# Kernel tuning notes

Hardware: AMD Instinct MI355X
Metric: run time of the kernel (lower is better)

## Reference

```python
import jax, jax.numpy as jnp
import numpy as np

SEQ, BATCH, IN_CH = 4096, 8, 256
HID = 256
LOOKBACK, LOOKAHEAD = 1, 0
K = LOOKBACK + 1 + LOOKAHEAD  # conv kernel size = 2


def setup_inputs() -> dict:
    key = jax.random.key(0)
    k1, k2, k3, k4, k5, k6 = jax.random.split(key, 6)
    X = jax.random.normal(k1, (SEQ, BATCH, IN_CH), dtype=jnp.float32)
    hidden = jax.random.normal(k2, (BATCH, HID), dtype=jnp.float32)
    scale = 1.0 / np.sqrt(IN_CH * K)
    Wz = jax.random.normal(k3, (HID, IN_CH, K), dtype=jnp.float32) * scale
    bz = jax.random.normal(k4, (HID,), dtype=jnp.float32) * scale
    Wf = jax.random.normal(k5, (HID, IN_CH, K), dtype=jnp.float32) * scale
    bf = jax.random.normal(k6, (HID,), dtype=jnp.float32) * scale
    return {"X": X, "hidden": hidden, "Wz": Wz, "bz": bz, "Wf": Wf, "bf": bf}


def _conv1d(Xp, W, b):
    # Xp: (B, C_in, S_pad); W: (C_out, C_in, K) -> (B, C_out, S)
    y = jax.lax.conv_general_dilated(
        Xp, W, window_strides=(1,), padding='VALID',
        dimension_numbers=('NCW', 'OIW', 'NCW'))
    return y + b[None, :, None]


def reference(X, hidden, Wz, bz, Wf, bf):
    # pad seq dim: lookback zeros in front, lookahead behind
    X_pad = jnp.pad(X, ((LOOKBACK, LOOKAHEAD), (0, 0), (0, 0)))
    Xp = jnp.transpose(X_pad, (1, 2, 0))  # (B, C_in, S_pad)

    Z = jnp.transpose(_conv1d(Xp, Wz, bz), (2, 0, 1))  # (S, B, H)
    F = jnp.transpose(_conv1d(Xp, Wf, bf), (2, 0, 1))  # (S, B, H)

    Z = Z * jax.nn.sigmoid(1.702 * Z)  # QuickGELU
    F = jax.nn.sigmoid(F)

    def step(h, fz):
        f, z = fz
        h = f * z + (1.0 - f) * h
        return h, h

    h_last, H = jax.lax.scan(step, hidden, (F, Z))
    return H, h_last[None]  # (S,B,H), (1,B,H)
```

## Files before the change

### kernel.cpp

```cpp
#include <hip/hip_runtime.h>


#define SEQn 4096
#define NCH 2048
#define CHUNK 32
#define NCHUNK 128

typedef __attribute__((ext_vector_type(8))) short bf16x8;
typedef __attribute__((ext_vector_type(4))) float floatx4;

__device__ __forceinline__ unsigned short f2bf(float x) {
  unsigned int u = __float_as_uint(x);
  u += 0x7fffu + ((u >> 16) & 1u);
  return (unsigned short)(u >> 16);
}
__device__ __forceinline__ float bf2f(ushort u) {
  return __uint_as_float((unsigned int)u << 16);
}
__device__ __forceinline__ float sigf(float x) {
  return __builtin_amdgcn_rcpf(1.0f + __expf(-x));
}

__global__ void pack_kernel(const float* __restrict__ X,
                            const float* __restrict__ Wz, const float* __restrict__ Wf,
                            ushort* __restrict__ Xbf, ushort* __restrict__ Bm) {
  if (blockIdx.x < 1024) {
    int idx = blockIdx.x * 256 + threadIdx.x;
    int n = idx >> 9, kin = idx & 511;
    const float* W = (n < 256) ? Wz : Wf;
    int h = n & 255, c = kin & 255, tap = kin >> 8;
    Bm[idx] = f2bf(W[h * 512 + c * 2 + tap]);
  } else {
    int idx = (blockIdx.x - 1024) * 256 + threadIdx.x;
    const int total4 = ((SEQn + 1) * NCH) / 4;
    if (idx >= total4) return;
    const int pad4 = NCH / 4;
    float4 v;
    if (idx < pad4) { v.x = 0.f; v.y = 0.f; v.z = 0.f; v.w = 0.f; }
    else v = ((const float4*)X)[idx - pad4];
    ushort4 o;
    o.x = f2bf(v.x); o.y = f2bf(v.y); o.z = f2bf(v.z); o.w = f2bf(v.w);
    ((ushort4*)Xbf)[idx] = o;
  }
}

__global__ __launch_bounds__(256) void gemm_kernel(
    const ushort* __restrict__ Xbf, const ushort* __restrict__ Bm,
    const float* __restrict__ bz, const float* __restrict__ bfb,
    ushort* __restrict__ zout, ushort* __restrict__ fout) {
  __shared__ __align__(16) char smem_raw[32768];
  ushort* sA = (ushort*)smem_raw;
  ushort* sB = (ushort*)(smem_raw + 16384);
  ushort* sT = (ushort*)smem_raw;

  const int tid  = threadIdx.x;
  const int wave = tid >> 6;
  const int lane = tid & 63;
  const int quad = lane >> 4;
  const int lrow = lane & 15;
  const int wm = wave >> 1;
  const int wn = wave & 1;
  const int bm = blockIdx.x;
  const int bn = blockIdx.y;

  floatx4 acc[4][4];
#pragma unroll
  for (int i = 0; i < 4; ++i)
#pragma unroll
    for (int j = 0; j < 4; ++j)
      acc[i][j] = (floatx4){0.f, 0.f, 0.f, 0.f};

  int rowS[4], gko[4];
#pragma unroll
  for (int it = 0; it < 4; ++it) {
    int g = wave * 256 + it * 64 + lane;
    int row = g >> 3, ks8 = g & 7;
    rowS[it] = row;
    gko[it] = (ks8 ^ (row & 7)) * 8;
  }
  char* ldsA = (char*)sA + wave * 4096 + (lane << 4);
  char* ldsB = (char*)sB + wave * 4096 + (lane << 4);

  for (int k0 = 0; k0 < 512; k0 += 64) {
    __syncthreads();
#pragma unroll
    for (int it = 0; it < 4; ++it) {
      const int kk = k0 + gko[it];
      const int cA = (kk < 256) ? kk : kk + 1792;
      __builtin_amdgcn_global_load_lds(
          (const __attribute__((address_space(1))) void*)(Xbf + (size_t)(bm * 128 + rowS[it]) * 256 + cA),
          (__attribute__((address_space(3))) void*)(ldsA + it * 1024), 16, 0, 0);
      __builtin_amdgcn_global_load_lds(
          (const __attribute__((address_space(1))) void*)(Bm + (size_t)(bn * 128 + rowS[it]) * 512 + kk),
          (__attribute__((address_space(3))) void*)(ldsB + it * 1024), 16, 0, 0);
    }
    __syncthreads();

    bf16x8 af[4][2], bfr[4][2];
#pragma unroll
    for (int fi = 0; fi < 4; ++fi) {
      const int r = wm * 64 + fi * 16 + lrow;
#pragma unroll
      for (int ks = 0; ks < 2; ++ks) {
        const int s = (ks * 4 + quad) ^ (r & 7);
        af[fi][ks] = *(const bf16x8*)&sA[r * 64 + s * 8];
      }
    }
#pragma unroll
    for (int fj = 0; fj < 4; ++fj) {
      const int r = wn * 64 + fj * 16 + lrow;
#pragma unroll
      for (int ks = 0; ks < 2; ++ks) {
        const int s = (ks * 4 + quad) ^ (r & 7);
        bfr[fj][ks] = *(const bf16x8*)&sB[r * 64 + s * 8];
      }
    }
#pragma unroll
    for (int ks = 0; ks < 2; ++ks)
#pragma unroll
      for (int fi = 0; fi < 4; ++fi)
#pragma unroll
        for (int fj = 0; fj < 4; ++fj)
          acc[fi][fj] = __builtin_amdgcn_mfma_f32_16x16x32_bf16(af[fi][ks], bfr[fj][ks], acc[fi][fj], 0, 0, 0);
  }

  const bool isZ = (bn < 2);
  ushort* gout = isZ ? zout : fout;
  const int ncol0 = (bn & 1) * 128;
  const float* bias = isZ ? bz : bfb;
  float bv[4];
#pragma unroll
  for (int fj = 0; fj < 4; ++fj)
    bv[fj] = bias[ncol0 + wn * 64 + fj * 16 + lrow];

  for (int round = 0; round < 2; ++round) {
    __syncthreads();
    if (wm == round) {
#pragma unroll
      for (int fi = 0; fi < 4; ++fi)
#pragma unroll
        for (int fj = 0; fj < 4; ++fj)
#pragma unroll
          for (int r = 0; r < 4; ++r) {
            float v = acc[fi][fj][r] + bv[fj];
            float o = isZ ? (v * sigf(1.702f * v)) : sigf(v);
            sT[(fi * 16 + quad * 4 + r) * 136 + wn * 64 + fj * 16 + lrow] = f2bf(o);
          }
    }
    __syncthreads();
#pragma unroll
    for (int it = 0; it < 4; ++it) {
      int e = tid + it * 256;
      int row = e >> 4, seg = e & 15;
      uint4 v = *(uint4*)&sT[row * 136 + seg * 8];
      *(uint4*)(gout + (size_t)(bm * 128 + round * 64 + row) * 256 + ncol0 + seg * 8) = v;
    }
  }
}

__global__ void scanA_kernel(const ushort* __restrict__ z, const ushort* __restrict__ f,
                             float* __restrict__ Ac, float* __restrict__ Cc) {
  int t = blockIdx.x * blockDim.x + threadIdx.x;
  int ch2 = t & 1023;
  int j = t >> 10;
  const size_t base = (size_t)j * CHUNK * NCH + 2 * ch2;
  const ushort* zp = z + base;
  const ushort* fp = f + base;
  float A0 = 1.0f, C0 = 0.0f, A1 = 1.0f, C1 = 0.0f;
#pragma unroll
  for (int i = 0; i < CHUNK; ++i) {
    ushort2 fv = *(const ushort2*)(fp + (size_t)i * NCH);
    ushort2 zv = *(const ushort2*)(zp + (size_t)i * NCH);
    float f0 = bf2f(fv.x), f1 = bf2f(fv.y);
    float a0 = 1.0f - f0, a1 = 1.0f - f1;
    C0 = fmaf(a0, C0, f0 * bf2f(zv.x)); A0 *= a0;
    C1 = fmaf(a1, C1, f1 * bf2f(zv.y)); A1 *= a1;
  }
  float2 Av = {A0, A1}, Cv = {C0, C1};
  *(float2*)(Ac + (size_t)j * NCH + 2 * ch2) = Av;
  *(float2*)(Cc + (size_t)j * NCH + 2 * ch2) = Cv;
}

__global__ void scanB_kernel(const float* __restrict__ hidden,
                             const float* __restrict__ Ac, const float* __restrict__ Cc,
                             float* __restrict__ Hs) {
  const int lane = threadIdx.x & 63;
  const int ch = blockIdx.x * 4 + (threadIdx.x >> 6);
  const int j0 = 2 * lane, j1 = 2 * lane + 1;
  float a0 = Ac[j0 * NCH + ch], c0 = Cc[j0 * NCH + ch];
  float a1 = Ac[j1 * NCH + ch], c1 = Cc[j1 * NCH + ch];
  float a = a0 * a1;
  float c = fmaf(a1, c0, c1);
#pragma unroll
  for (int d = 1; d < 64; d <<= 1) {
    float pa = __shfl_up(a, d, 64);
    float pc = __shfl_up(c, d, 64);
    if (lane >= d) { c = fmaf(a, pc, c); a *= pa; }
  }
  float xa = __shfl_up(a, 1, 64), xc = __shfl_up(c, 1, 64);
  if (lane == 0) { xa = 1.0f; xc = 0.0f; }
  float h0 = hidden[ch];
  float hs0 = fmaf(xa, h0, xc);
  Hs[j0 * NCH + ch] = hs0;
  Hs[j1 * NCH + ch] = fmaf(a0, hs0, c0);
}

__global__ void scanC_kernel(const ushort* __restrict__ z, const ushort* __restrict__ f,
                             const float* __restrict__ Hs, float* __restrict__ out) {
  int t = blockIdx.x * blockDim.x + threadIdx.x;
  int ch2 = t & 1023;
  int j = t >> 10;
  float2 hv = *(const float2*)(Hs + (size_t)j * NCH + 2 * ch2);
  float h0 = hv.x, h1 = hv.y;
  const size_t base = (size_t)j * CHUNK * NCH + 2 * ch2;
  const ushort* zp = z + base;
  const ushort* fp = f + base;
  float* op = out + base;
#pragma unroll
  for (int i = 0; i < CHUNK; ++i) {
    ushort2 fv = *(const ushort2*)(fp + (size_t)i * NCH);
    ushort2 zv = *(const ushort2*)(zp + (size_t)i * NCH);
    float f0 = bf2f(fv.x), f1 = bf2f(fv.y);
    h0 = fmaf(f0, bf2f(zv.x) - h0, h0);
    h1 = fmaf(f1, bf2f(zv.y) - h1, h1);
    float2 o = {h0, h1};
    *(float2*)(op + (size_t)i * NCH) = o;
  }
  if (j == NCHUNK - 1) {
    float2 o = {h0, h1};
    *(float2*)(out + (size_t)SEQn * NCH + 2 * ch2) = o;
  }
}

extern "C" void kernel_launch(void* const* d_in, const int* in_sizes, int n_in,
                              void* d_out, int out_size, void* d_ws, size_t ws_size,
                              hipStream_t stream) {
  const float* X      = (const float*)d_in[0];
  const float* hidden = (const float*)d_in[1];
  const float* Wz     = (const float*)d_in[2];
  const float* bz     = (const float*)d_in[3];
  const float* Wf     = (const float*)d_in[4];
  const float* bfb    = (const float*)d_in[5];
  float* out = (float*)d_out;

  char* ws = (char*)d_ws;
  ushort* zbf = (ushort*)ws;
  ushort* fbf = (ushort*)(ws + 16777216);
  ushort* Xbf = (ushort*)(ws + 33554432);
  ushort* Bm  = (ushort*)(ws + 50335744);
  float* Ac = (float*)(ws + 33554432);
  float* Cc = (float*)(ws + 34603008);
  float* Hs = (float*)(ws + 35651584);

  pack_kernel<<<9218, 256, 0, stream>>>(X, Wz, Wf, Xbf, Bm);
  dim3 ggrid(256, 4);
  gemm_kernel<<<ggrid, 256, 0, stream>>>(Xbf, Bm, bz, bfb, zbf, fbf);
  scanA_kernel<<<512, 256, 0, stream>>>(zbf, fbf, Ac, Cc);
  scanB_kernel<<<512, 256, 0, stream>>>(hidden, Ac, Cc, Hs);
  scanC_kernel<<<512, 256, 0, stream>>>(zbf, fbf, Hs, out);
}
```

Measured before the change: 144.4 us.

## Fuse three scan passes into one persistent kernel with grid barriers

Merges the chunk-reduce, cross-chunk prefix, and chunk-apply scan kernels into a single 512-block kernel separated by atomic grid-wide barriers. The z/f values for each chunk stay in registers between the first and third phases, so they are not re-read from global memory, and two kernel launches are removed. The risks are higher register pressure from the 64 cached words, barrier spin overhead, and a possible deadlock if all 512 blocks cannot be co-resident. The barrier counter is reset inside the pack kernel.

```diff
diff --git a/kernel.cpp b/kernel.cpp
--- a/kernel.cpp
+++ b/kernel.cpp
@@ -5,6 +5,7 @@
 #define NCH 2048
 #define CHUNK 32
 #define NCHUNK 128
+#define NBLK_SCAN 512
 
 typedef __attribute__((ext_vector_type(8))) short bf16x8;
 typedef __attribute__((ext_vector_type(4))) float floatx4;
@@ -17,13 +18,35 @@
 __device__ __forceinline__ float bf2f(ushort u) {
   return __uint_as_float((unsigned int)u << 16);
 }
+__device__ __forceinline__ float bf2f_lo(unsigned int v) {
+  return __uint_as_float(v << 16);
+}
+__device__ __forceinline__ float bf2f_hi(unsigned int v) {
+  return __uint_as_float(v & 0xffff0000u);
+}
 __device__ __forceinline__ float sigf(float x) {
   return __builtin_amdgcn_rcpf(1.0f + __expf(-x));
 }
 
+__device__ __forceinline__ void grid_bar(unsigned int* bar, unsigned int target) {
+  __syncthreads();
+  if (threadIdx.x == 0) {
+    __threadfence();
+    __hip_atomic_fetch_add(bar, 1u, __ATOMIC_RELEASE, __HIP_MEMORY_SCOPE_AGENT);
+    while (__hip_atomic_load(bar, __ATOMIC_ACQUIRE, __HIP_MEMORY_SCOPE_AGENT) < target) {
+      __builtin_amdgcn_s_sleep(2);
+    }
+    __threadfence();
+  }
+  __syncthreads();
+}
+
 __global__ void pack_kernel(const float* __restrict__ X,
                             const float* __restrict__ Wz, const float* __restrict__ Wf,
-                            ushort* __restrict__ Xbf, ushort* __restrict__ Bm) {
+                            ushort* __restrict__ Xbf, ushort* __restrict__ Bm,
+                            unsigned int* __restrict__ bar) {
+  if (blockIdx.x == 0 && threadIdx.x == 0)
+    __hip_atomic_store(bar, 0u, __ATOMIC_RELAXED, __HIP_MEMORY_SCOPE_AGENT);
   if (blockIdx.x < 1024) {
     int idx = blockIdx.x * 256 + threadIdx.x;
     int n = idx >> 9, kin = idx & 511;
@@ -158,77 +181,77 @@
   }
 }
 
-__global__ void scanA_kernel(const ushort* __restrict__ z, const ushort* __restrict__ f,
-                             float* __restrict__ Ac, float* __restrict__ Cc) {
-  int t = blockIdx.x * blockDim.x + threadIdx.x;
-  int ch2 = t & 1023;
-  int j = t >> 10;
+__global__ __launch_bounds__(256, 2) void scan_fused(
+    const float* __restrict__ hidden,
+    const ushort* __restrict__ z, const ushort* __restrict__ f,
+    float* __restrict__ Ac, float* __restrict__ Cc, float* __restrict__ Hs,
+    float* __restrict__ out, unsigned int* __restrict__ bar) {
+  const int t = blockIdx.x * 256 + threadIdx.x;
+  const int ch2 = t & 1023;
+  const int j = t >> 10;
   const size_t base = (size_t)j * CHUNK * NCH + 2 * ch2;
-  const ushort* zp = z + base;
-  const ushort* fp = f + base;
+
+  unsigned int zreg[CHUNK], freg[CHUNK];
   float A0 = 1.0f, C0 = 0.0f, A1 = 1.0f, C1 = 0.0f;
 #pragma unroll
   for (int i = 0; i < CHUNK; ++i) {
-    ushort2 fv = *(const ushort2*)(fp + (size_t)i * NCH);
-    ushort2 zv = *(const ushort2*)(zp + (size_t)i * NCH);
-    float f0 = bf2f(fv.x), f1 = bf2f(fv.y);
+    unsigned int fv = *(const unsigned int*)(f + base + (size_t)i * NCH);
+    unsigned int zv = *(const unsigned int*)(z + base + (size_t)i * NCH);
+    freg[i] = fv; zreg[i] = zv;
+    float f0 = bf2f_lo(fv), f1 = bf2f_hi(fv);
     float a0 = 1.0f - f0, a1 = 1.0f - f1;
-    C0 = fmaf(a0, C0, f0 * bf2f(zv.x)); A0 *= a0;
-    C1 = fmaf(a1, C1, f1 * bf2f(zv.y)); A1 *= a1;
-  }
-  float2 Av = {A0, A1}, Cv = {C0, C1};
-  *(float2*)(Ac + (size_t)j * NCH + 2 * ch2) = Av;
-  *(float2*)(Cc + (size_t)j * NCH + 2 * ch2) = Cv;
-}
-
-__global__ void scanB_kernel(const float* __restrict__ hidden,
-                             const float* __restrict__ Ac, const float* __restrict__ Cc,
-                             float* __restrict__ Hs) {
-  const int lane = threadIdx.x & 63;
-  const int ch = blockIdx.x * 4 + (threadIdx.x >> 6);
-  const int j0 = 2 * lane, j1 = 2 * lane + 1;
-  float a0 = Ac[j0 * NCH + ch], c0 = Cc[j0 * NCH + ch];
-  float a1 = Ac[j1 * NCH + ch], c1 = Cc[j1 * NCH + ch];
-  float a = a0 * a1;
-  float c = fmaf(a1, c0, c1);
-#pragma unroll
-  for (int d = 1; d < 64; d <<= 1) {
-    float pa = __shfl_up(a, d, 64);
-    float pc = __shfl_up(c, d, 64);
-    if (lane >= d) { c = fmaf(a, pc, c); a *= pa; }
-  }
-  float xa = __shfl_up(a, 1, 64), xc = __shfl_up(c, 1, 64);
-  if (lane == 0) { xa = 1.0f; xc = 0.0f; }
-  float h0 = hidden[ch];
-  float hs0 = fmaf(xa, h0, xc);
-  Hs[j0 * NCH + ch] = hs0;
-  Hs[j1 * NCH + ch] = fmaf(a0, hs0, c0);
-}
-
-__global__ void scanC_kernel(const ushort* __restrict__ z, const ushort* __restrict__ f,
-                             const float* __restrict__ Hs, float* __restrict__ out) {
-  int t = blockIdx.x * blockDim.x + threadIdx.x;
-  int ch2 = t & 1023;
-  int j = t >> 10;
-  float2 hv = *(const float2*)(Hs + (size_t)j * NCH + 2 * ch2);
-  float h0 = hv.x, h1 = hv.y;
-  const size_t base = (size_t)j * CHUNK * NCH + 2 * ch2;
-  const ushort* zp = z + base;
-  const ushort* fp = f + base;
-  float* op = out + base;
-#pragma unroll
-  for (int i = 0; i < CHUNK; ++i) {
-    ushort2 fv = *(const ushort2*)(fp + (size_t)i * NCH);
-    ushort2 zv = *(const ushort2*)(zp + (size_t)i * NCH);
-    float f0 = bf2f(fv.x), f1 = bf2f(fv.y);
-    h0 = fmaf(f0, bf2f(zv.x) - h0, h0);
-    h1 = fmaf(f1, bf2f(zv.y) - h1, h1);
-    float2 o = {h0, h1};
-    *(float2*)(op + (size_t)i * NCH) = o;
-  }
-  if (j == NCHUNK - 1) {
-    float2 o = {h0, h1};
-    *(float2*)(out + (size_t)SEQn * NCH + 2 * ch2) = o;
+    C0 = fmaf(a0, C0, f0 * bf2f_lo(zv)); A0 *= a0;
+    C1 = fmaf(a1, C1, f1 * bf2f_hi(zv)); A1 *= a1;
+  }
+  {
+    float2 Av = {A0, A1}, Cv = {C0, C1};
+    *(float2*)(Ac + (size_t)j * NCH + 2 * ch2) = Av;
+    *(float2*)(Cc + (size_t)j * NCH + 2 * ch2) = Cv;
+  }
+
+  grid_bar(bar, NBLK_SCAN);
+
+  {
+    const int lane = threadIdx.x & 63;
+    const int ch = blockIdx.x * 4 + (threadIdx.x >> 6);
+    const int j0 = 2 * lane, j1 = 2 * lane + 1;
+    float a0 = Ac[j0 * NCH + ch], c0 = Cc[j0 * NCH + ch];
+    float a1 = Ac[j1 * NCH + ch], c1 = Cc[j1 * NCH + ch];
+    float a = a0 * a1;
+    float c = fmaf(a1, c0, c1);
+#pragma unroll
+    for (int d = 1; d < 64; d <<= 1) {
+      float pa = __shfl_up(a, d, 64);
+      float pc = __shfl_up(c, d, 64);
+      if (lane >= d) { c = fmaf(a, pc, c); a *= pa; }
+    }
+    float xa = __shfl_up(a, 1, 64), xc = __shfl_up(c, 1, 64);
+    if (lane == 0) { xa = 1.0f; xc = 0.0f; }
+    float h0 = hidden[ch];
+    float hs0 = fmaf(xa, h0, xc);
+    Hs[j0 * NCH + ch] = hs0;
+    Hs[j1 * NCH + ch] = fmaf(a0, hs0, c0);
+  }
+
+  grid_bar(bar, 2 * NBLK_SCAN);
+
+  {
+    float2 hv = *(const float2*)(Hs + (size_t)j * NCH + 2 * ch2);
+    float h0 = hv.x, h1 = hv.y;
+    float* op = out + base;
+#pragma unroll
+    for (int i = 0; i < CHUNK; ++i) {
+      unsigned int fv = freg[i], zv = zreg[i];
+      float f0 = bf2f_lo(fv), f1 = bf2f_hi(fv);
+      h0 = fmaf(f0, bf2f_lo(zv) - h0, h0);
+      h1 = fmaf(f1, bf2f_hi(zv) - h1, h1);
+      float2 o = {h0, h1};
+      *(float2*)(op + (size_t)i * NCH) = o;
+    }
+    if (j == NCHUNK - 1) {
+      float2 o = {h0, h1};
+      *(float2*)(out + (size_t)SEQn * NCH + 2 * ch2) = o;
+    }
   }
 }
 
@@ -248,14 +271,13 @@
   ushort* fbf = (ushort*)(ws + 16777216);
   ushort* Xbf = (ushort*)(ws + 33554432);
   ushort* Bm  = (ushort*)(ws + 50335744);
+  unsigned int* bar = (unsigned int*)(ws + 50860032);
   float* Ac = (float*)(ws + 33554432);
   float* Cc = (float*)(ws + 34603008);
   float* Hs = (float*)(ws + 35651584);
 
-  pack_kernel<<<9218, 256, 0, stream>>>(X, Wz, Wf, Xbf, Bm);
+  pack_kernel<<<9218, 256, 0, stream>>>(X, Wz, Wf, Xbf, Bm, bar);
   dim3 ggrid(256, 4);
   gemm_kernel<<<ggrid, 256, 0, stream>>>(Xbf, Bm, bz, bfb, zbf, fbf);
-  scanA_kernel<<<512, 256, 0, stream>>>(zbf, fbf, Ac, Cc);
-  scanB_kernel<<<512, 256, 0, stream>>>(hidden, Ac, Cc, Hs);
-  scanC_kernel<<<512, 256, 0, stream>>>(zbf, fbf, Hs, out);
-}
+  scan_fused<<<512, 256, 0, stream>>>(hidden, zbf, fbf, Ac, Cc, Hs, out, bar);
+}
```

New measurement: 287.5 us. 99.1% more time.

## Double-buffer LDS tiles in GEMM to overlap global loads with MFMA

Applied to the files above, without the earlier changes.

Doubles shared memory in the conv-as-GEMM kernel to two 32KB stages and issues the next k-tile's global_load_lds before computing the current tile. This drops one barrier per k-step and aims to hide global memory latency behind the matrix multiplies. The cost is 64KB of LDS per block, which may lower occupancy. Correctness relies on the single barrier at the end of each iteration covering both the load completion and the buffer reuse.

```diff
diff --git a/kernel.cpp b/kernel.cpp
--- a/kernel.cpp
+++ b/kernel.cpp
@@ -48,9 +48,7 @@
     const ushort* __restrict__ Xbf, const ushort* __restrict__ Bm,
     const float* __restrict__ bz, const float* __restrict__ bfb,
     ushort* __restrict__ zout, ushort* __restrict__ fout) {
-  __shared__ __align__(16) char smem_raw[32768];
-  ushort* sA = (ushort*)smem_raw;
-  ushort* sB = (ushort*)(smem_raw + 16384);
+  __shared__ __align__(16) char smem_raw[65536];
   ushort* sT = (ushort*)smem_raw;
 
   const int tid  = threadIdx.x;
@@ -78,23 +76,36 @@
     rowS[it] = row;
     gko[it] = (ks8 ^ (row & 7)) * 8;
   }
-  char* ldsA = (char*)sA + wave * 4096 + (lane << 4);
-  char* ldsB = (char*)sB + wave * 4096 + (lane << 4);
-
-  for (int k0 = 0; k0 < 512; k0 += 64) {
-    __syncthreads();
-#pragma unroll
-    for (int it = 0; it < 4; ++it) {
-      const int kk = k0 + gko[it];
-      const int cA = (kk < 256) ? kk : kk + 1792;
-      __builtin_amdgcn_global_load_lds(
-          (const __attribute__((address_space(1))) void*)(Xbf + (size_t)(bm * 128 + rowS[it]) * 256 + cA),
-          (__attribute__((address_space(3))) void*)(ldsA + it * 1024), 16, 0, 0);
-      __builtin_amdgcn_global_load_lds(
-          (const __attribute__((address_space(1))) void*)(Bm + (size_t)(bn * 128 + rowS[it]) * 512 + kk),
-          (__attribute__((address_space(3))) void*)(ldsB + it * 1024), 16, 0, 0);
-    }
-    __syncthreads();
+
+  const ushort* Arow = Xbf + (size_t)(bm * 128) * 256;
+  const ushort* Brow = Bm + (size_t)(bn * 128) * 512;
+
+#define STAGE(curb, k0)                                                          \
+  {                                                                              \
+    char* lA = smem_raw + (curb) * 32768 + wave * 4096 + (lane << 4);            \
+    char* lB = lA + 16384;                                                       \
+    _Pragma("unroll")                                                            \
+    for (int it = 0; it < 4; ++it) {                                             \
+      const int kk = (k0) + gko[it];                                             \
+      const int cA = (kk < 256) ? kk : kk + 1792;      \
+      __builtin_amdgcn_global_load_lds(                                          \
+          (const __attribute__((address_space(1))) void*)(Arow + (size_t)rowS[it] * 256 + cA), \
+          (__attribute__((address_space(3))) void*)(lA + it * 1024), 16, 0, 0);  \
+      __builtin_amdgcn_global_load_lds(                                          \
+          (const __attribute__((address_space(1))) void*)(Brow + (size_t)rowS[it] * 512 + kk), \
+          (__attribute__((address_space(3))) void*)(lB + it * 1024), 16, 0, 0);  \
+    }                                                                            \
+  }
+
+  STAGE(0, 0);
+  __syncthreads();
+
+  int cur = 0;
+  for (int t = 0; t < 8; ++t) {
+    if (t < 7) STAGE(cur ^ 1, (t + 1) * 64);
+
+    const ushort* sA = (const ushort*)(smem_raw + cur * 32768);
+    const ushort* sB = sA + 8192;
 
     bf16x8 af[4][2], bfr[4][2];
 #pragma unroll
@@ -122,7 +133,11 @@
 #pragma unroll
         for (int fj = 0; fj < 4; ++fj)
           acc[fi][fj] = __builtin_amdgcn_mfma_f32_16x16x32_bf16(af[fi][ks], bfr[fj][ks], acc[fi][fj], 0, 0, 0);
-  }
+
+    __syncthreads();
+    cur ^= 1;
+  }
+#undef STAGE
 
   const bool isZ = (bn < 2);
   ushort* gout = isZ ? zout : fout;
```

New measurement: 153.8 us. +6.5%, slower.

## Retile GEMM to 64x256 blocks with 8 waves covering full Z/F width

Applied to the files above, without the earlier changes.

The GEMM kernel moves from 128x128 tiles with 4 waves to 64x256 tiles with 8 waves. Each block now computes a full 256-column Z or F slice for 64 rows, and the grid changes to 1024 one-dimensional blocks. This cuts redundant A-tile loads (A is read once per Z/F rather than twice) and simplifies the epilogue into a single pass. In exchange, B loads per block double, each wave holds fewer accumulators, and LDS use grows to 40KB, which may change occupancy.

```diff
diff --git a/kernel.cpp b/kernel.cpp
--- a/kernel.cpp
+++ b/kernel.cpp
@@ -44,13 +44,13 @@
   }
 }
 
-__global__ __launch_bounds__(256) void gemm_kernel(
+__global__ __launch_bounds__(512) void gemm_kernel(
     const ushort* __restrict__ Xbf, const ushort* __restrict__ Bm,
     const float* __restrict__ bz, const float* __restrict__ bfb,
     ushort* __restrict__ zout, ushort* __restrict__ fout) {
-  __shared__ __align__(16) char smem_raw[32768];
+  __shared__ __align__(16) char smem_raw[40960];
   ushort* sA = (ushort*)smem_raw;
-  ushort* sB = (ushort*)(smem_raw + 16384);
+  ushort* sB = sA + 4096;
   ushort* sT = (ushort*)smem_raw;
 
   const int tid  = threadIdx.x;
@@ -58,48 +58,54 @@
   const int lane = tid & 63;
   const int quad = lane >> 4;
   const int lrow = lane & 15;
-  const int wm = wave >> 1;
-  const int wn = wave & 1;
-  const int bm = blockIdx.x;
-  const int bn = blockIdx.y;
-
-  floatx4 acc[4][4];
+  const int id = blockIdx.x;
+  const int bnZF = id >> 9;
+  const int bm = id & 511;
+
+  floatx4 acc[4][2];
 #pragma unroll
   for (int i = 0; i < 4; ++i)
 #pragma unroll
-    for (int j = 0; j < 4; ++j)
+    for (int j = 0; j < 2; ++j)
       acc[i][j] = (floatx4){0.f, 0.f, 0.f, 0.f};
 
-  int rowS[4], gko[4];
+  const int rowA = tid >> 3;
+  const int gkoA = ((tid & 7) ^ (rowA & 7)) * 8;
+  int rowBG[4], gkoB[4];
 #pragma unroll
   for (int it = 0; it < 4; ++it) {
-    int g = wave * 256 + it * 64 + lane;
-    int row = g >> 3, ks8 = g & 7;
-    rowS[it] = row;
-    gko[it] = (ks8 ^ (row & 7)) * 8;
-  }
-  char* ldsA = (char*)sA + wave * 4096 + (lane << 4);
-  char* ldsB = (char*)sB + wave * 4096 + (lane << 4);
+    int g = it * 512 + tid;
+    int row = g >> 3, s = g & 7;
+    rowBG[it] = bnZF * 256 + row;
+    gkoB[it] = (s ^ (row & 7)) * 8;
+  }
+  char* ldsA = smem_raw + (tid << 4);
+  char* ldsB = smem_raw + 8192 + (tid << 4);
+
+  const ushort* Arow = Xbf + (size_t)(bm * 64) * 256;
 
   for (int k0 = 0; k0 < 512; k0 += 64) {
     __syncthreads();
-#pragma unroll
-    for (int it = 0; it < 4; ++it) {
-      const int kk = k0 + gko[it];
+    {
+      const int kk = k0 + gkoA;
       const int cA = (kk < 256) ? kk : kk + 1792;
       __builtin_amdgcn_global_load_lds(
-          (const __attribute__((address_space(1))) void*)(Xbf + (size_t)(bm * 128 + rowS[it]) * 256 + cA),
-          (__attribute__((address_space(3))) void*)(ldsA + it * 1024), 16, 0, 0);
+          (const __attribute__((address_space(1))) void*)(Arow + (size_t)rowA * 256 + cA),
+          (__attribute__((address_space(3))) void*)ldsA, 16, 0, 0);
+    }
+#pragma unroll
+    for (int it = 0; it < 4; ++it) {
+      const int kk = k0 + gkoB[it];
       __builtin_amdgcn_global_load_lds(
-          (const __attribute__((address_space(1))) void*)(Bm + (size_t)(bn * 128 + rowS[it]) * 512 + kk),
-          (__attribute__((address_space(3))) void*)(ldsB + it * 1024), 16, 0, 0);
+          (const __attribute__((address_space(1))) void*)(Bm + (size_t)rowBG[it] * 512 + kk),
+          (__attribute__((address_space(3))) void*)(ldsB + it * 8192), 16, 0, 0);
     }
     __syncthreads();
 
-    bf16x8 af[4][2], bfr[4][2];
+    bf16x8 af[4][2], bfr[2][2];
 #pragma unroll
     for (int fi = 0; fi < 4; ++fi) {
-      const int r = wm * 64 + fi * 16 + lrow;
+      const int r = fi * 16 + lrow;
 #pragma unroll
       for (int ks = 0; ks < 2; ++ks) {
         const int s = (ks * 4 + quad) ^ (r & 7);
@@ -107,8 +113,8 @@
       }
     }
 #pragma unroll
-    for (int fj = 0; fj < 4; ++fj) {
-      const int r = wn * 64 + fj * 16 + lrow;
+    for (int fj = 0; fj < 2; ++fj) {
+      const int r = wave * 32 + fj * 16 + lrow;
 #pragma unroll
       for (int ks = 0; ks < 2; ++ks) {
         const int s = (ks * 4 + quad) ^ (r & 7);
@@ -120,41 +126,35 @@
 #pragma unroll
       for (int fi = 0; fi < 4; ++fi)
 #pragma unroll
-        for (int fj = 0; fj < 4; ++fj)
+        for (int fj = 0; fj < 2; ++fj)
           acc[fi][fj] = __builtin_amdgcn_mfma_f32_16x16x32_bf16(af[fi][ks], bfr[fj][ks], acc[fi][fj], 0, 0, 0);
   }
 
-  const bool isZ = (bn < 2);
-  ushort* gout = isZ ? zout : fout;
-  const int ncol0 = (bn & 1) * 128;
-  const float* bias = isZ ? bz : bfb;
-  float bv[4];
-#pragma unroll
-  for (int fj = 0; fj < 4; ++fj)
-    bv[fj] = bias[ncol0 + wn * 64 + fj * 16 + lrow];
-
-  for (int round = 0; round < 2; ++round) {
-    __syncthreads();
-    if (wm == round) {
-#pragma unroll
-      for (int fi = 0; fi < 4; ++fi)
-#pragma unroll
-        for (int fj = 0; fj < 4; ++fj)
-#pragma unroll
-          for (int r = 0; r < 4; ++r) {
-            float v = acc[fi][fj][r] + bv[fj];
-            float o = isZ ? (v * sigf(1.702f * v)) : sigf(v);
-            sT[(fi * 16 + quad * 4 + r) * 136 + wn * 64 + fj * 16 + lrow] = f2bf(o);
-          }
-    }
-    __syncthreads();
-#pragma unroll
-    for (int it = 0; it < 4; ++it) {
-      int e = tid + it * 256;
-      int row = e >> 4, seg = e & 15;
-      uint4 v = *(uint4*)&sT[row * 136 + seg * 8];
-      *(uint4*)(gout + (size_t)(bm * 128 + round * 64 + row) * 256 + ncol0 + seg * 8) = v;
-    }
+  ushort* gout = bnZF ? fout : zout;
+  const float* bias = bnZF ? bfb : bz;
+  float bv[2];
+#pragma unroll
+  for (int fj = 0; fj < 2; ++fj)
+    bv[fj] = bias[wave * 32 + fj * 16 + lrow];
+
+  __syncthreads();
+#pragma unroll
+  for (int fi = 0; fi < 4; ++fi)
+#pragma unroll
+    for (int fj = 0; fj < 2; ++fj)
+#pragma unroll
+      for (int r = 0; r < 4; ++r) {
+        float v = acc[fi][fj][r] + bv[fj];
+        float o = bnZF ? sigf(v) : (v * sigf(1.702f * v));
+        sT[(fi * 16 + quad * 4 + r) * 264 + wave * 32 + fj * 16 + lrow] = f2bf(o);
+      }
+  __syncthreads();
+#pragma unroll
+  for (int it = 0; it < 4; ++it) {
+    int e = tid + it * 512;
+    int row = e >> 5, seg = e & 31;
+    uint4 v = *(uint4*)&sT[row * 264 + seg * 8];
+    *(uint4*)(gout + (size_t)(bm * 64 + row) * 256 + seg * 8) = v;
   }
 }
 
@@ -253,8 +253,7 @@
   float* Hs = (float*)(ws + 35651584);
 
   pack_kernel<<<9218, 256, 0, stream>>>(X, Wz, Wf, Xbf, Bm);
-  dim3 ggrid(256, 4);
-  gemm_kernel<<<ggrid, 256, 0, stream>>>(Xbf, Bm, bz, bfb, zbf, fbf);
+  gemm_kernel<<<1024, 512, 0, stream>>>(Xbf, Bm, bz, bfb, zbf, fbf);
   scanA_kernel<<<512, 256, 0, stream>>>(zbf, fbf, Ac, Cc);
   scanB_kernel<<<512, 256, 0, stream>>>(hidden, Ac, Cc, Hs);
   scanC_kernel<<<512, 256, 0, stream>>>(zbf, fbf, Hs, out);
```

New measurement: 140.6 us. 1.03x faster.
